# Performance work log

Hardware: AMD Instinct MI355X
Metric: run time of the kernel (lower is better)

## Reference

```python
import jax, jax.numpy as jnp
import numpy as np

N = 100000   # nodes
E = 1600000  # edges (avg degree 16)
D = 128      # embed_dim
H1, C1 = 8, 16   # gat1: heads=8, out=embed_dim//8=16, concat -> 128
C2 = 32          # gat2: heads=1, out=32
NEG_SLOPE = 0.2  # PyG GATConv default leaky relu slope


def _gat_layer(x, src, dst, W, a_src, a_dst, b, heads, ch, concat):
    """PyG-style GATConv (eval mode, add_self_loops already applied via src/dst)."""
    n = x.shape[0]
    h = (x @ W).reshape(n, heads, ch)                      # [N,H,C]
    alpha_s = jnp.einsum('nhc,hc->nh', h, a_src)           # [N,H]
    alpha_d = jnp.einsum('nhc,hc->nh', h, a_dst)           # [N,H]
    e = jax.nn.leaky_relu(alpha_s[src] + alpha_d[dst], NEG_SLOPE)  # [Etot,H]
    # segment softmax over incoming edges of each dst node
    m = jax.ops.segment_max(e, dst, num_segments=n)        # [N,H]
    ex = jnp.exp(e - m[dst])
    s = jax.ops.segment_sum(ex, dst, num_segments=n)       # [N,H]
    alpha = ex / (s[dst] + 1e-16)                          # [Etot,H]
    out = jax.ops.segment_sum(alpha[:, :, None] * h[src], dst, num_segments=n)  # [N,H,C]
    out = out.reshape(n, heads * ch) if concat else out.mean(axis=1)
    return out + b


def setup_inputs():
    key = jax.random.key(0)
    ks = jax.random.split(key, 12)
    x = jax.random.normal(ks[0], (N, D), dtype=jnp.float32)
    edge_index = jax.random.randint(ks[1], (2, E), 0, N, dtype=jnp.int64)
    sc = 0.1
    W1 = jax.random.normal(ks[2], (D, H1 * C1), jnp.float32) * sc
    a1_src = jax.random.normal(ks[3], (H1, C1), jnp.float32) * sc
    a1_dst = jax.random.normal(ks[4], (H1, C1), jnp.float32) * sc
    b1 = jnp.zeros((H1 * C1,), jnp.float32)
    W2 = jax.random.normal(ks[5], (H1 * C1, C2), jnp.float32) * sc
    a2_src = jax.random.normal(ks[6], (1, C2), jnp.float32) * sc
    a2_dst = jax.random.normal(ks[7], (1, C2), jnp.float32) * sc
    b2 = jnp.zeros((C2,), jnp.float32)
    Wh = jax.random.normal(ks[8], (C2, 1), jnp.float32) * sc
    bh = jnp.zeros((1,), jnp.float32)
    return {"x": x, "edge_index": edge_index,
            "W1": W1, "a1_src": a1_src, "a1_dst": a1_dst, "b1": b1,
            "W2": W2, "a2_src": a2_src, "a2_dst": a2_dst, "b2": b2,
            "Wh": Wh, "bh": bh}


def reference(x, edge_index, W1, a1_src, a1_dst, b1, W2, a2_src, a2_dst, b2, Wh, bh):
    n = x.shape[0]
    loops = jnp.arange(n, dtype=edge_index.dtype)
    src = jnp.concatenate([edge_index[0], loops])  # add_self_loops=True (PyG default)
    dst = jnp.concatenate([edge_index[1], loops])
    h = jax.nn.elu(_gat_layer(x, src, dst, W1, a1_src, a1_dst, b1, H1, C1, True))
    h = jax.nn.elu(_gat_layer(h, src, dst, W2, a2_src, a2_dst, b2, 1, C2, False))
    return h @ Wh + bh  # [N,1] ordinal head
```

## Files before the change

kernel.cpp:

```cpp
#include <hip/hip_runtime.h>
#include <hip/hip_bf16.h>
#include <stdint.h>
#include <stddef.h>

#define NEG_SLOPE 0.2f
#define XS 136

#define NBK   196
#define BWSH  9
#define BCAP  12288
#define NPREP 64

typedef __bf16 bf16x8 __attribute__((ext_vector_type(8)));
typedef float  f32x4  __attribute__((ext_vector_type(4)));

__device__ __forceinline__ float bf2f(__hip_bfloat16 b){ return __bfloat162float(b); }
__device__ __forceinline__ float lo_bf(unsigned u){ return __uint_as_float(u << 16); }
__device__ __forceinline__ float hi_bf(unsigned u){ return __uint_as_float(u & 0xffff0000u); }
__device__ __forceinline__ float lrelu(float u){ return fmaxf(u, NEG_SLOPE * u); }
__device__ __forceinline__ unsigned short f2bf(float f){
    unsigned u = __float_as_uint(f);
    return (unsigned short)((u + 0x7fffu + ((u >> 16) & 1u)) >> 16);
}
__device__ __forceinline__ float bfs2f(unsigned short s){ return __uint_as_float((unsigned)s << 16); }
__device__ __forceinline__ float ldraw(const void* p, int i, int isf){
    return isf ? ((const float*)p)[i] : bf2f(((const __hip_bfloat16*)p)[i]);
}

__global__ void detect_kernel(const unsigned* __restrict__ ei,
                              const unsigned* __restrict__ xw,
                              int* __restrict__ flags,
                              int* __restrict__ gcur){
    __shared__ int vote;
    const int t = threadIdx.x;
    if (t == 0) vote = 0;
    if (t < NBK) gcur[t] = t * BCAP;
    __syncthreads();
    if (t < 64){
        unsigned long long m = __ballot(ei[2*t + 1] != 0u);
        if (t == 0) flags[0] = (m == 0ull) ? 1 : 0;
    }
    {
        unsigned lo = xw[t] & 0xffffu;
        unsigned e  = (lo >> 7) & 0xffu;
        int pl = ((lo & 0x7fffu) == 0u || (e >= 100u && e <= 140u)) ? 1 : 0;
        atomicAdd(&vote, pl);
    }
    __syncthreads();
    if (t == 0) flags[1] = (vote < 128) ? 1 : 0;
}

#define WTS_TOTAL 20993
__global__ __launch_bounds__(256) void prep_scatter_kernel(
        const void* __restrict__ ei, const int* __restrict__ flags,
        int* __restrict__ gcur, unsigned* __restrict__ pairs, int E, int Et, int nsb,
        const void* W1, const void* W2, const void* a1s, const void* a1d,
        const void* b1, const void* a2s, const void* a2d, const void* b2,
        const void* Wh, const void* bh,
        float* __restrict__ w, unsigned short* __restrict__ w1x,
        unsigned short* __restrict__ w2x){
    const int t = threadIdx.x;
    if ((int)blockIdx.x < nsb){
        __shared__ int cnt[NBK], base[NBK], lcnt[NBK];
        const int e0 = blockIdx.x * 4096;
        const int nE = min(4096, Et - e0);
        for (int i = t; i < NBK; i += 256){ cnt[i] = 0; lcnt[i] = 0; }
        __syncthreads();
        const int is64 = flags[0];
        int2 sd[16];
#pragma unroll
        for (int k = 0; k < 16; k++){
            int j = t + k * 256;
            if (j < nE){
                int e = e0 + j, s, d;
                if (e >= E){ s = e - E; d = s; }
                else if (is64){
                    const long long* p = (const long long*)ei;
                    s = (int)p[e]; d = (int)p[(size_t)E + e];
                } else {
                    const int* p = (const int*)ei;
                    s = p[e]; d = p[(size_t)E + e];
                }
                sd[k] = make_int2(s, d);
                atomicAdd(&cnt[d >> BWSH], 1);
            } else sd[k].y = -1;
        }
        __syncthreads();
        for (int b = t; b < NBK; b += 256)
            base[b] = cnt[b] ? atomicAdd(&gcur[b], cnt[b]) : 0;
        __syncthreads();
#pragma unroll
        for (int k = 0; k < 16; k++){
            if (sd[k].y >= 0){
                int b = sd[k].y >> BWSH;
                int r = atomicAdd(&lcnt[b], 1);
                pairs[(size_t)base[b] + r] = ((unsigned)sd[k].x << BWSH) | (unsigned)(sd[k].y & 511);
            }
        }
    } else {
        const int p   = blockIdx.x - nsb;
        const int tid = p * 256 + t;
        const int NT  = NPREP * 256;
        const int isf = flags[1];
        for (int i = tid; i < 513; i += NT){
            int gi = 20480 + i;
            const void* src; int off;
            if      (gi < 20608){ src = a1s; off = gi - 20480; }
            else if (gi < 20736){ src = a1d; off = gi - 20608; }
            else if (gi < 20864){ src = b1;  off = gi - 20736; }
            else if (gi < 20896){ src = a2s; off = gi - 20864; }
            else if (gi < 20928){ src = a2d; off = gi - 20896; }
            else if (gi < 20960){ src = b2;  off = gi - 20928; }
            else if (gi < 20992){ src = Wh;  off = gi - 20960; }
            else                { src = bh;  off = 0; }
            w[gi] = ldraw(src, off, isf);
        }
        for (int i = tid; i < 16384; i += NT){
            int c = i >> 7, k = i & 127;
            w1x[i] = f2bf(ldraw(W1, k*128 + c, isf));
        }
        for (int i = tid; i < 4096; i += NT){
            int c = i >> 7, k = i & 127;
            w2x[i] = f2bf(ldraw(W2, k*32 + c, isf));
        }
        for (int i = tid; i < 12*128; i += NT) w2x[36*128 + i] = 0;
        for (int i = tid; i < 1024; i += NT){
            int h = i >> 7, k = i & 127;
            float ss = 0.f, dd = 0.f;
#pragma unroll
            for (int j = 0; j < 16; j++){
                float hv = ldraw(W1, k*128 + h*16 + j, isf);
                ss += hv * ldraw(a1s, h*16 + j, isf);
                dd += hv * ldraw(a1d, h*16 + j, isf);
            }
            unsigned short sh = f2bf(ss), dh = f2bf(dd);
            w1x[(128+h)*128 + k] = sh;
            w1x[(136+h)*128 + k] = f2bf(ss - bfs2f(sh));
            w1x[(144+h)*128 + k] = dh;
            w1x[(152+h)*128 + k] = f2bf(dd - bfs2f(dh));
        }
        for (int k = tid; k < 128; k += NT){
            float ss = 0.f, dd = 0.f;
#pragma unroll
            for (int j = 0; j < 32; j++){
                float hv = ldraw(W2, k*32 + j, isf);
                ss += hv * ldraw(a2s, j, isf);
                dd += hv * ldraw(a2d, j, isf);
            }
            unsigned short sh = f2bf(ss), dh = f2bf(dd);
            w2x[32*128 + k] = sh;
            w2x[33*128 + k] = f2bf(ss - bfs2f(sh));
            w2x[34*128 + k] = dh;
            w2x[35*128 + k] = f2bf(dd - bfs2f(dh));
        }
    }
}

__global__ __launch_bounds__(256) void g1csr_kernel(
        const unsigned* __restrict__ pairs, const int* __restrict__ gcur,
        int* __restrict__ rowptr, int* __restrict__ csr_src, int Nn,
        const void* __restrict__ xv, const unsigned short* __restrict__ w1x,
        const int* __restrict__ flags, __hip_bfloat16* __restrict__ h1b,
        float* __restrict__ as1, float* __restrict__ ad1){
    __shared__ __align__(16) char smem[52224];
    const int t = threadIdx.x;
    if ((int)blockIdx.x < NBK){
        int* ssz   = (int*)smem;
        int* sscan = ssz + 256;
        int* cnt   = sscan + 256;
        int* sh    = cnt + 512;
        const int b = blockIdx.x;
        int v = (t < NBK) ? (gcur[t] - t * BCAP) : 0;
        ssz[t] = v; sscan[t] = v;
        __syncthreads();
        for (int off = 1; off < 256; off <<= 1){
            int x = (t >= off) ? sscan[t - off] : 0;
            __syncthreads();
            sscan[t] += x;
            __syncthreads();
        }
        const int sz = ssz[b];
        const int eb = (b == 0) ? 0 : sscan[b - 1];
        if (b == 0 && t == 0) rowptr[Nn] = sscan[NBK - 1];
        const unsigned* pp = pairs + (size_t)b * BCAP;
        cnt[t] = 0; cnt[t + 256] = 0;
        __syncthreads();
        for (int i = t; i < sz; i += 256) atomicAdd(&cnt[pp[i] & 511u], 1);
        __syncthreads();
        int l0 = 2*t, l1 = 2*t + 1;
        int s0 = cnt[l0], s1 = cnt[l1], ts = s0 + s1;
        sh[t] = ts; __syncthreads();
        for (int off = 1; off < 256; off <<= 1){
            int x = (t >= off) ? sh[t - off] : 0;
            __syncthreads();
            sh[t] += x;
            __syncthreads();
        }
        int excl = sh[t] - ts;
        __syncthreads();
        cnt[l0] = eb + excl;
        cnt[l1] = eb + excl + s0;
        int n0 = (b << BWSH) + l0, n1 = (b << BWSH) + l1;
        if (n0 < Nn) rowptr[n0] = cnt[l0];
        if (n1 < Nn) rowptr[n1] = cnt[l1];
        __syncthreads();
        for (int i = t; i < sz; i += 256){
            unsigned sd = pp[i];
            int pos = atomicAdd(&cnt[sd & 511u], 1);
            csr_src[pos] = (int)(sd >> BWSH);
        }
    } else {
        __bf16* xls = (__bf16*)smem;
        __bf16* wls = (__bf16*)(smem + 64 * XS * 2);
        const int row0 = ((int)blockIdx.x - NBK) * 64;
        const int n = Nn;

#pragma unroll
        for (int k = 0; k < 8; k++){
            int e = (t + k * 256) * 8;
            int c = e >> 7, kk = e & 127;
            *(uint4*)(&wls[c * XS + kk]) = *(const uint4*)(w1x + e);
        }
        if (row0 + 64 <= n){
            if (flags[1]){
                const float* xp = (const float*)xv + (size_t)row0 * 128;
#pragma unroll
                for (int k = 0; k < 8; k++){
                    int e = (t + k * 256) * 4;
                    int row = e >> 7, col = e & 127;
                    float4 vv = *(const float4*)(xp + e);
                    uint2 o;
                    o.x = (unsigned)f2bf(vv.x) | ((unsigned)f2bf(vv.y) << 16);
                    o.y = (unsigned)f2bf(vv.z) | ((unsigned)f2bf(vv.w) << 16);
                    *(uint2*)(&xls[row * XS + col]) = o;
                }
            } else {
                const unsigned short* xp = (const unsigned short*)xv + (size_t)row0 * 128;
#pragma unroll
                for (int k = 0; k < 4; k++){
                    int e = (t + k * 256) * 8;
                    int row = e >> 7, col = e & 127;
                    *(uint4*)(&xls[row * XS + col]) = *(const uint4*)(xp + e);
                }
            }
        } else {
            const int limit = (n - row0) * 128;
            if (flags[1]){
                const float* xp = (const float*)xv + (size_t)row0 * 128;
                for (int i = t; i < 64 * 128; i += 256){
                    float v = (i < limit) ? xp[i] : 0.f;
                    xls[(i >> 7) * XS + (i & 127)] = (__bf16)v;
                }
            } else {
                const unsigned short* xp = (const unsigned short*)xv + (size_t)row0 * 128;
                for (int i = t; i < 64 * 128; i += 256){
                    unsigned short v = (i < limit) ? xp[i] : (unsigned short)0;
                    ((unsigned short*)xls)[(i >> 7) * XS + (i & 127)] = v;
                }
            }
        }
        __syncthreads();

        const int w    = t >> 6;
        const int lane = t & 63;
        const int l15  = lane & 15;
        const int quad = lane >> 4;

        f32x4 acc[8] = {};
        f32x4 accS = {}, accD = {};
        const __bf16* xbase = &xls[(w * 16 + l15) * XS + quad * 8];
        const __bf16* wbase = &wls[l15 * XS + quad * 8];
        const unsigned short* vsrow = w1x + (128 + l15) * 128 + quad * 8;
        const unsigned short* vdrow = w1x + (144 + l15) * 128 + quad * 8;

#pragma unroll
        for (int ks = 0; ks < 4; ks++){
            bf16x8 af = *(const bf16x8*)(xbase + ks * 32);
#pragma unroll
            for (int tt = 0; tt < 8; tt++){
                bf16x8 bfr = *(const bf16x8*)(wbase + tt * 16 * XS + ks * 32);
                acc[tt] = __builtin_amdgcn_mfma_f32_16x16x32_bf16(af, bfr, acc[tt], 0, 0, 0);
            }
            bf16x8 bS = *(const bf16x8*)(vsrow + ks * 32);
            bf16x8 bD = *(const bf16x8*)(vdrow + ks * 32);
            accS = __builtin_amdgcn_mfma_f32_16x16x32_bf16(af, bS, accS, 0, 0, 0);
            accD = __builtin_amdgcn_mfma_f32_16x16x32_bf16(af, bD, accD, 0, 0, 0);
        }

#pragma unroll
        for (int tt = 0; tt < 8; tt++){
            int col = tt * 16 + l15;
#pragma unroll
            for (int r = 0; r < 4; r++){
                int row = row0 + w * 16 + quad * 4 + r;
                if (row < n) h1b[(size_t)row * 128 + col] = __float2bfloat16(acc[tt][r]);
            }
        }
#pragma unroll
        for (int r = 0; r < 4; r++){
            float vs = accS[r] + __shfl_xor(accS[r], 8);
            float vd = accD[r] + __shfl_xor(accD[r], 8);
            int row = row0 + w * 16 + quad * 4 + r;
            if (l15 < 8 && row < n){
                as1[(size_t)row * 8 + l15] = vs;
                ad1[(size_t)row * 8 + l15] = vd;
            }
        }
    }
}

__global__ __launch_bounds__(256) void gather1_kernel(const int* __restrict__ rowptr,
                                                      const int* __restrict__ csr_src,
                                                      const float* __restrict__ as1,
                                                      const float* __restrict__ ad1,
                                                      const unsigned* __restrict__ h1u,
                                                      const float* __restrict__ b1,
                                                      unsigned* __restrict__ out1u, int n){
    int wid = blockIdx.x * 4 + (threadIdx.x >> 6);
    if (wid >= n) return;
    const int lane = threadIdx.x & 63;
    const int q    = lane >> 4;
    const int l15  = lane & 15;
    const int h    = l15 >> 1;
    const int start = rowptr[wid], end = rowptr[wid + 1];
    const float adv = ad1[(size_t)wid * 8 + h];
    float den = 0.f;
    float num[8] = {0.f,0.f,0.f,0.f,0.f,0.f,0.f,0.f};
    for (int j = start + q; j < end; j += 4){
        int src = csr_src[j];
        float u = lrelu(as1[(size_t)src * 8 + h] + adv);
        float w = __expf(u);
        uint4 hv = *(const uint4*)(h1u + (size_t)src * 64 + (l15 << 2));
        den += w;
        num[0] += w * lo_bf(hv.x); num[1] += w * hi_bf(hv.x);
        num[2] += w * lo_bf(hv.y); num[3] += w * hi_bf(hv.y);
        num[4] += w * lo_bf(hv.z); num[5] += w * hi_bf(hv.z);
        num[6] += w * lo_bf(hv.w); num[7] += w * hi_bf(hv.w);
    }
    den += __shfl_xor(den, 16); den += __shfl_xor(den, 32);
#pragma unroll
    for (int k = 0; k < 8; k++){
        num[k] += __shfl_xor(num[k], 16);
        num[k] += __shfl_xor(num[k], 32);
    }
    if (lane < 16){
        const int ch0 = l15 * 8;
        float inv = 1.f / (den + 1e-16f);
        uint4 o;
        unsigned* op = (unsigned*)&o;
#pragma unroll
        for (int k = 0; k < 4; k++){
            float r0 = num[2*k]   * inv + b1[ch0 + 2*k];
            float r1 = num[2*k+1] * inv + b1[ch0 + 2*k + 1];
            r0 = r0 > 0.f ? r0 : __expf(r0) - 1.f;
            r1 = r1 > 0.f ? r1 : __expf(r1) - 1.f;
            op[k] = (unsigned)f2bf(r0) | ((unsigned)f2bf(r1) << 16);
        }
        *(uint4*)(out1u + (size_t)wid * 64 + (l15 << 2)) = o;
    }
}

__global__ __launch_bounds__(256) void gemm2_kernel(const unsigned* __restrict__ out1u,
                                                    const unsigned short* __restrict__ w2x,
                                                    __hip_bfloat16* __restrict__ h2b,
                                                    float* __restrict__ as2,
                                                    float* __restrict__ ad2, int n){
    __shared__ __align__(16) __bf16 als[64 * XS];
    __shared__ __align__(16) __bf16 wls[32 * XS];
    const int t = threadIdx.x;
    const int row0 = blockIdx.x * 64;

#pragma unroll
    for (int k = 0; k < 2; k++){
        int e = (t + k * 256) * 8;
        int c = e >> 7, kk = e & 127;
        *(uint4*)(&wls[c * XS + kk]) = *(const uint4*)(w2x + e);
    }
    if (row0 + 64 <= n){
#pragma unroll
        for (int k = 0; k < 4; k++){
            int e = (t + k * 256) * 4;
            int row = e >> 6, cu = e & 63;
            *(uint4*)(&((unsigned*)als)[row * 68 + cu]) =
                *(const uint4*)(out1u + (size_t)row0 * 64 + e);
        }
    } else {
        const int limit = (n - row0) * 64;
        for (int i = t; i < 64 * 64; i += 256){
            unsigned v = (i < limit) ? out1u[(size_t)row0 * 64 + i] : 0u;
            ((unsigned*)als)[(i >> 6) * 68 + (i & 63)] = v;
        }
    }
    __syncthreads();

    const int w    = t >> 6;
    const int lane = t & 63;
    const int l15  = lane & 15;
    const int quad = lane >> 4;

    f32x4 acc[2] = {};
    f32x4 accE = {};
    const __bf16* abase = &als[(w * 16 + l15) * XS + quad * 8];
    const __bf16* bbase = &wls[l15 * XS + quad * 8];
    const unsigned short* verow = w2x + (32 + l15) * 128 + quad * 8;

#pragma unroll
    for (int ks = 0; ks < 4; ks++){
        bf16x8 af = *(const bf16x8*)(abase + ks * 32);
#pragma unroll
        for (int tt = 0; tt < 2; tt++){
            bf16x8 bfr = *(const bf16x8*)(bbase + tt * 16 * XS + ks * 32);
            acc[tt] = __builtin_amdgcn_mfma_f32_16x16x32_bf16(af, bfr, acc[tt], 0, 0, 0);
        }
        bf16x8 bE = *(const bf16x8*)(verow + ks * 32);
        accE = __builtin_amdgcn_mfma_f32_16x16x32_bf16(af, bE, accE, 0, 0, 0);
    }

#pragma unroll
    for (int r = 0; r < 4; r++){
        int row = row0 + w * 16 + quad * 4 + r;
        if (row < n){
#pragma unroll
            for (int tt = 0; tt < 2; tt++){
                int col = tt * 16 + l15;
                h2b[(size_t)row * 32 + col] = __float2bfloat16(acc[tt][r]);
            }
        }
        float vE = accE[r] + __shfl_xor(accE[r], 1);
        if (row < n){
            if (l15 == 0) as2[row] = vE;
            if (l15 == 2) ad2[row] = vE;
        }
    }
}

__global__ __launch_bounds__(256) void gather2_kernel(const int* __restrict__ rowptr,
                                                      const int* __restrict__ csr_src,
                                                      const float* __restrict__ as2,
                                                      const float* __restrict__ ad2,
                                                      const unsigned* __restrict__ h2u,
                                                      const float* __restrict__ b2,
                                                      const float* __restrict__ Wh,
                                                      const float* __restrict__ bh,
                                                      const int* __restrict__ flags,
                                                      void* __restrict__ out, int n){
    int wid = blockIdx.x * 4 + (threadIdx.x >> 6);
    if (wid >= n) return;
    int lane = threadIdx.x & 63;
    int q    = lane >> 4;
    int i2   = lane & 15;
    int ch0  = i2 * 2;
    int start = rowptr[wid], end = rowptr[wid + 1];
    float adv = ad2[wid];
    float den = 0.f, num0 = 0.f, num1 = 0.f;
    for (int j = start + q; j < end; j += 4){
        int src = csr_src[j];
        float u = lrelu(as2[src] + adv);
        float w = __expf(u);
        unsigned hv = h2u[(size_t)src * 16 + i2];
        den += w;
        num0 += w * lo_bf(hv);
        num1 += w * hi_bf(hv);
    }
    den  += __shfl_xor(den, 16);  den  += __shfl_xor(den, 32);
    num0 += __shfl_xor(num0, 16); num0 += __shfl_xor(num0, 32);
    num1 += __shfl_xor(num1, 16); num1 += __shfl_xor(num1, 32);
    float inv = 1.f / (den + 1e-16f);
    float v0 = num0 * inv + b2[ch0];
    float v1 = num1 * inv + b2[ch0 + 1];
    v0 = v0 > 0.f ? v0 : __expf(v0) - 1.f;
    v1 = v1 > 0.f ? v1 : __expf(v1) - 1.f;
    float p = v0 * Wh[ch0] + v1 * Wh[ch0 + 1];
#pragma unroll
    for (int off = 1; off < 16; off <<= 1) p += __shfl_xor(p, off);
    if (lane == 0){
        float r = p + bh[0];
        if (flags[1]) ((float*)out)[wid] = r;
        else          ((__hip_bfloat16*)out)[wid] = __float2bfloat16(r);
    }
}

extern "C" void kernel_launch(void* const* d_in, const int* in_sizes, int n_in,
                              void* d_out, int out_size, void* d_ws, size_t ws_size,
                              hipStream_t stream){
    const void* x   = d_in[0];
    const void* ei  = d_in[1];

    const int Nn = in_sizes[0] / 128;
    const int Ee = in_sizes[1] / 2;
    const int Et = Ee + Nn;
    const int nsb = (Et + 4095) / 4096;

    char* ws = (char*)d_ws;
    auto al = [](size_t v){ return (v + 255) & ~(size_t)255; };
    size_t off = 0;
    int*      flags  = (int*)(ws + off);      off = al(off + 16);
    float*    wts    = (float*)(ws + off);    off = al(off + (size_t)WTS_TOTAL * 4);
    unsigned short* w1x = (unsigned short*)(ws + off); off = al(off + 160 * 128 * 2);
    unsigned short* w2x = (unsigned short*)(ws + off); off = al(off + 48 * 128 * 2);
    int*      gcur   = (int*)(ws + off);      off = al(off + (size_t)NBK * 4);
    int*      rowptr = (int*)(ws + off);      off = al(off + (size_t)(Nn + 1) * 4);
    int*      csrs   = (int*)(ws + off);      off = al(off + (size_t)Et * 4);
    unsigned* pairs  = (unsigned*)(ws + off); off = al(off + (size_t)NBK * BCAP * 4);
    size_t o_h1 = off;
    __hip_bfloat16* h1b = (__hip_bfloat16*)(ws + off); off = al(off + (size_t)Nn * 128 * 2);
    float* as1  = (float*)(ws + off); off = al(off + (size_t)Nn * 8 * 4);
    float* ad1  = (float*)(ws + off); off = al(off + (size_t)Nn * 8 * 4);
    unsigned* out1u = (unsigned*)(ws + off); off = al(off + (size_t)Nn * 128 * 2);
    size_t o2 = o_h1;
    __hip_bfloat16* h2b = (__hip_bfloat16*)(ws + o2); o2 += (size_t)Nn * 32 * 2;
    float* as2  = (float*)(ws + o2);  o2 += (size_t)Nn * 4;
    float* ad2  = (float*)(ws + o2);  o2 += (size_t)Nn * 4;

    float* b1f  = wts + 20736;
    float* b2f  = wts + 20928;
    float* Whf  = wts + 20960;
    float* bhf  = wts + 20992;

    detect_kernel<<<1, 256, 0, stream>>>((const unsigned*)ei, (const unsigned*)x, flags, gcur);

    prep_scatter_kernel<<<nsb + NPREP, 256, 0, stream>>>(ei, flags, gcur, pairs, Ee, Et, nsb,
        d_in[2], d_in[6], d_in[3], d_in[4], d_in[5], d_in[7], d_in[8], d_in[9],
        d_in[10], d_in[11], wts, w1x, w2x);

    g1csr_kernel<<<NBK + (Nn + 63) / 64, 256, 0, stream>>>(pairs, gcur, rowptr, csrs, Nn,
        x, w1x, flags, h1b, as1, ad1);

    gather1_kernel<<<(Nn + 3) / 4, 256, 0, stream>>>(rowptr, csrs, as1, ad1,
                                                     (const unsigned*)h1b, b1f, out1u, Nn);

    gemm2_kernel<<<(Nn + 63) / 64, 256, 0, stream>>>(out1u, w2x, h2b, as2, ad2, Nn);

    gather2_kernel<<<(Nn + 3) / 4, 256, 0, stream>>>(rowptr, csrs, as2, ad2,
                                                     (const unsigned*)h2b, b2f,
                                                     Whf, bhf, flags, d_out, Nn);
}
```

Before: 313.2 us.

## Remap gather lanes to process more edges per wave with wider loads and prefetch

Both gather kernels change how the 64 lanes of a wavefront are split between edges and channels. Layer 1 now handles 8 edges at once, with one lane per head doing two 16-byte loads. Layer 2 handles 16 edges at once, with each lane doing one 16-byte load. The next edge's source index is prefetched one iteration ahead and the loop is unrolled by 2, so the index load overlaps the feature gather. More edges in flight per wave targets the memory latency of average-degree-16 rows, at the cost of more registers per lane, an extra shuffle-reduction step, and fewer active lanes in the epilogue.

```diff
diff --git a/kernel.cpp b/kernel.cpp
--- a/kernel.cpp
+++ b/kernel.cpp
@@ -319,44 +319,70 @@
     int wid = blockIdx.x * 4 + (threadIdx.x >> 6);
     if (wid >= n) return;
     const int lane = threadIdx.x & 63;
-    const int q    = lane >> 4;
-    const int l15  = lane & 15;
-    const int h    = l15 >> 1;
+    const int g    = lane >> 3;
+    const int h    = lane & 7;
     const int start = rowptr[wid], end = rowptr[wid + 1];
     const float adv = ad1[(size_t)wid * 8 + h];
     float den = 0.f;
-    float num[8] = {0.f,0.f,0.f,0.f,0.f,0.f,0.f,0.f};
-    for (int j = start + q; j < end; j += 4){
-        int src = csr_src[j];
-        float u = lrelu(as1[(size_t)src * 8 + h] + adv);
-        float w = __expf(u);
-        uint4 hv = *(const uint4*)(h1u + (size_t)src * 64 + (l15 << 2));
-        den += w;
-        num[0] += w * lo_bf(hv.x); num[1] += w * hi_bf(hv.x);
-        num[2] += w * lo_bf(hv.y); num[3] += w * hi_bf(hv.y);
-        num[4] += w * lo_bf(hv.z); num[5] += w * hi_bf(hv.z);
-        num[6] += w * lo_bf(hv.w); num[7] += w * hi_bf(hv.w);
-    }
-    den += __shfl_xor(den, 16); den += __shfl_xor(den, 32);
-#pragma unroll
-    for (int k = 0; k < 8; k++){
+    float num[16] = {0.f,0.f,0.f,0.f,0.f,0.f,0.f,0.f,
+                     0.f,0.f,0.f,0.f,0.f,0.f,0.f,0.f};
+    int j   = start + g;
+    int src = (j < end) ? csr_src[j] : -1;
+    const int iters = (end - start + 7) >> 3;
+#pragma unroll 2
+    for (int it = 0; it < iters; ++it){
+        const int jn   = j + 8;
+        const int srcn = (jn < end) ? csr_src[jn] : -1;
+        if (src >= 0){
+            const unsigned* hp = h1u + (size_t)src * 64 + h * 8;
+            uint4 hv0 = *(const uint4*)(hp);
+            uint4 hv1 = *(const uint4*)(hp + 4);
+            float u = lrelu(as1[src * 8 + h] + adv);
+            float w = __expf(u);
+            den += w;
+            num[0]  += w * lo_bf(hv0.x); num[1]  += w * hi_bf(hv0.x);
+            num[2]  += w * lo_bf(hv0.y); num[3]  += w * hi_bf(hv0.y);
+            num[4]  += w * lo_bf(hv0.z); num[5]  += w * hi_bf(hv0.z);
+            num[6]  += w * lo_bf(hv0.w); num[7]  += w * hi_bf(hv0.w);
+            num[8]  += w * lo_bf(hv1.x); num[9]  += w * hi_bf(hv1.x);
+            num[10] += w * lo_bf(hv1.y); num[11] += w * hi_bf(hv1.y);
+            num[12] += w * lo_bf(hv1.z); num[13] += w * hi_bf(hv1.z);
+            num[14] += w * lo_bf(hv1.w); num[15] += w * hi_bf(hv1.w);
+        }
+        j = jn; src = srcn;
+    }
+    den += __shfl_xor(den, 8); den += __shfl_xor(den, 16); den += __shfl_xor(den, 32);
+#pragma unroll
+    for (int k = 0; k < 16; k++){
+        num[k] += __shfl_xor(num[k], 8);
         num[k] += __shfl_xor(num[k], 16);
         num[k] += __shfl_xor(num[k], 32);
     }
-    if (lane < 16){
-        const int ch0 = l15 * 8;
+    if (g == 0){
+        const int ch0 = h * 16;
         float inv = 1.f / (den + 1e-16f);
-        uint4 o;
-        unsigned* op = (unsigned*)&o;
-#pragma unroll
-        for (int k = 0; k < 4; k++){
-            float r0 = num[2*k]   * inv + b1[ch0 + 2*k];
-            float r1 = num[2*k+1] * inv + b1[ch0 + 2*k + 1];
+        uint4 o0, o1;
+        unsigned* op0 = (unsigned*)&o0;
+        unsigned* op1 = (unsigned*)&o1;
+#pragma unroll
+        for (int m = 0; m < 4; m++){
+            float r0 = num[2*m]   * inv + b1[ch0 + 2*m];
+            float r1 = num[2*m+1] * inv + b1[ch0 + 2*m + 1];
             r0 = r0 > 0.f ? r0 : __expf(r0) - 1.f;
             r1 = r1 > 0.f ? r1 : __expf(r1) - 1.f;
-            op[k] = (unsigned)f2bf(r0) | ((unsigned)f2bf(r1) << 16);
-        }
-        *(uint4*)(out1u + (size_t)wid * 64 + (l15 << 2)) = o;
+            op0[m] = (unsigned)f2bf(r0) | ((unsigned)f2bf(r1) << 16);
+        }
+#pragma unroll
+        for (int m = 4; m < 8; m++){
+            float r0 = num[2*m]   * inv + b1[ch0 + 2*m];
+            float r1 = num[2*m+1] * inv + b1[ch0 + 2*m + 1];
+            r0 = r0 > 0.f ? r0 : __expf(r0) - 1.f;
+            r1 = r1 > 0.f ? r1 : __expf(r1) - 1.f;
+            op1[m - 4] = (unsigned)f2bf(r0) | ((unsigned)f2bf(r1) << 16);
+        }
+        unsigned* ob = out1u + (size_t)wid * 64 + h * 8;
+        *(uint4*)(ob)     = o0;
+        *(uint4*)(ob + 4) = o1;
     }
 }
 
@@ -446,33 +472,53 @@
                                                       void* __restrict__ out, int n){
     int wid = blockIdx.x * 4 + (threadIdx.x >> 6);
     if (wid >= n) return;
-    int lane = threadIdx.x & 63;
-    int q    = lane >> 4;
-    int i2   = lane & 15;
-    int ch0  = i2 * 2;
-    int start = rowptr[wid], end = rowptr[wid + 1];
-    float adv = ad2[wid];
-    float den = 0.f, num0 = 0.f, num1 = 0.f;
-    for (int j = start + q; j < end; j += 4){
-        int src = csr_src[j];
-        float u = lrelu(as2[src] + adv);
-        float w = __expf(u);
-        unsigned hv = h2u[(size_t)src * 16 + i2];
-        den += w;
-        num0 += w * lo_bf(hv);
-        num1 += w * hi_bf(hv);
-    }
-    den  += __shfl_xor(den, 16);  den  += __shfl_xor(den, 32);
-    num0 += __shfl_xor(num0, 16); num0 += __shfl_xor(num0, 32);
-    num1 += __shfl_xor(num1, 16); num1 += __shfl_xor(num1, 32);
-    float inv = 1.f / (den + 1e-16f);
-    float v0 = num0 * inv + b2[ch0];
-    float v1 = num1 * inv + b2[ch0 + 1];
-    v0 = v0 > 0.f ? v0 : __expf(v0) - 1.f;
-    v1 = v1 > 0.f ? v1 : __expf(v1) - 1.f;
-    float p = v0 * Wh[ch0] + v1 * Wh[ch0 + 1];
-#pragma unroll
-    for (int off = 1; off < 16; off <<= 1) p += __shfl_xor(p, off);
+    const int lane = threadIdx.x & 63;
+    const int g = lane >> 2;
+    const int c = lane & 3;
+    const int start = rowptr[wid], end = rowptr[wid + 1];
+    const float adv = ad2[wid];
+    float den = 0.f;
+    float num[8] = {0.f,0.f,0.f,0.f,0.f,0.f,0.f,0.f};
+    int j   = start + g;
+    int src = (j < end) ? csr_src[j] : -1;
+    const int iters = (end - start + 15) >> 4;
+#pragma unroll 2
+    for (int it = 0; it < iters; ++it){
+        const int jn   = j + 16;
+        const int srcn = (jn < end) ? csr_src[jn] : -1;
+        if (src >= 0){
+            uint4 hv = *(const uint4*)(h2u + (size_t)src * 16 + c * 4);
+            float u = lrelu(as2[src] + adv);
+            float w = __expf(u);
+            den += w;
+            num[0] += w * lo_bf(hv.x); num[1] += w * hi_bf(hv.x);
+            num[2] += w * lo_bf(hv.y); num[3] += w * hi_bf(hv.y);
+            num[4] += w * lo_bf(hv.z); num[5] += w * hi_bf(hv.z);
+            num[6] += w * lo_bf(hv.w); num[7] += w * hi_bf(hv.w);
+        }
+        j = jn; src = srcn;
+    }
+    den += __shfl_xor(den, 4); den += __shfl_xor(den, 8);
+    den += __shfl_xor(den, 16); den += __shfl_xor(den, 32);
+#pragma unroll
+    for (int k = 0; k < 8; k++){
+        num[k] += __shfl_xor(num[k], 4);
+        num[k] += __shfl_xor(num[k], 8);
+        num[k] += __shfl_xor(num[k], 16);
+        num[k] += __shfl_xor(num[k], 32);
+    }
+    float p = 0.f;
+    if (g == 0){
+        const int ch0 = c * 8;
+        float inv = 1.f / (den + 1e-16f);
+#pragma unroll
+        for (int k = 0; k < 8; k++){
+            float v = num[k] * inv + b2[ch0 + k];
+            v = v > 0.f ? v : __expf(v) - 1.f;
+            p += v * Wh[ch0 + k];
+        }
+    }
+    p += __shfl_xor(p, 1); p += __shfl_xor(p, 2);
     if (lane == 0){
         float r = p + bh[0];
         if (flags[1]) ((float*)out)[wid] = r;
```

After: 296.6 us. 1.06x faster.
